# Optimization experiments

Measured on AMD Instinct MI355X. Metric: run time of the kernel, lower is better.

## Reference

```python
import jax, jax.numpy as jnp
import numpy as np

TOP_K = 30
NUM_RBF = 16
EDGE_F = 128
NODE_F = 128
MAXREL = 32
EDGE_IN = NUM_RBF * 25  # 400


def _normalize(x, eps=1e-12):
    n = jnp.linalg.norm(x, axis=-1, keepdims=True)
    return x / jnp.maximum(n, eps)


def _rbf(D):
    # D: [..., ] distances -> [..., NUM_RBF]
    mu = jnp.linspace(2.0, 22.0, NUM_RBF)
    sigma = (22.0 - 2.0) / NUM_RBF
    return jnp.exp(-(((D[..., None] - mu) / sigma) ** 2))


def _layer_norm(x, g, b, eps=1e-5):
    m = x.mean(-1, keepdims=True)
    v = ((x - m) ** 2).mean(-1, keepdims=True)
    return (x - m) / jnp.sqrt(v + eps) * g + b


def setup_inputs() -> dict:
    key = jax.random.key(0)
    ks = jax.random.split(key, 8)
    B, L = 8, 1024
    X = jax.random.normal(ks[0], (B, L, 5, 3), jnp.float32) * 3.0  # backbone coords
    mask = jnp.ones((B, L), jnp.float32)
    Lvec = jnp.full((B,), L, dtype=jnp.int32)
    W_edge = jax.random.normal(ks[1], (EDGE_IN, EDGE_F), jnp.float32) * 0.05
    W_node = jax.random.normal(ks[2], (6, NODE_F), jnp.float32) * 0.05
    W_pos = jax.random.normal(ks[3], (2 * MAXREL + 1, EDGE_F), jnp.float32) * 0.05
    b_pos = jnp.zeros((EDGE_F,), jnp.float32)
    g_edge = jnp.ones((EDGE_F,), jnp.float32)
    b_edge = jnp.zeros((EDGE_F,), jnp.float32)
    g_node = jnp.ones((NODE_F,), jnp.float32)
    b_node = jnp.zeros((NODE_F,), jnp.float32)
    return {"X": X, "mask": mask, "Lvec": Lvec, "W_edge": W_edge, "W_node": W_node,
            "W_pos": W_pos, "b_pos": b_pos, "g_edge": g_edge, "b_edge": b_edge,
            "g_node": g_node, "b_node": b_node}


def reference(X, mask, Lvec, W_edge, W_node, W_pos, b_pos, g_edge, b_edge, g_node, b_node):
    B, L = X.shape[0], X.shape[1]
    N, Ca, C, CB, O = (X[:, :, i, :] for i in range(5))

    # backbone frames (4x4: rotation rows e1,e2,e3; translation Ca; bottom row zeros)
    v1 = C - Ca
    v2 = N - Ca
    e1 = _normalize(v1)
    u2 = v2 - e1 * jnp.sum(e1 * v2, axis=-1, keepdims=True)
    e2 = _normalize(u2)
    e3 = jnp.cross(e1, e2)
    R = jnp.stack([e1, e2, e3], axis=-2)  # [B,L,3,3]
    bb = jnp.zeros((B, L, 4, 4), X.dtype).at[..., :3, :3].set(R).at[..., :3, 3].set(Ca)

    # _dist: masked Ca-Ca pairwise distance + kNN
    mask2 = mask[:, None, :] * mask[:, :, None]  # [B,L,L]
    dX = Ca[:, :, None, :] - Ca[:, None, :, :]
    D = mask2 * jnp.sqrt(jnp.sum(dX ** 2, -1) + 1e-6)
    D_max = jnp.max(D, -1, keepdims=True)
    D_adjust = D + (1.0 - mask2) * D_max
    k = min(TOP_K, L)
    negD, E_idx = jax.lax.top_k(-D_adjust, k)  # smallest-k distances
    D_neighbors = -negD  # [B,L,K]

    # RBFs: compute distances only at selected neighbors (same math as full cdist+gather)
    bidx = jnp.arange(B)[:, None, None]

    def get_rbf(A, Bc):
        Bnb = Bc[bidx, E_idx]  # [B,L,K,3]
        d = jnp.sqrt(jnp.sum((A[:, :, None, :] - Bnb) ** 2, -1) + 1e-6)
        return _rbf(d)

    pairs = [(N, N), (C, C), (O, O), (CB, CB), (Ca, N), (Ca, C), (Ca, O), (Ca, CB),
             (N, C), (N, O), (N, CB), (CB, C), (CB, O), (O, C), (N, Ca), (C, Ca),
             (O, Ca), (CB, Ca), (C, N), (O, N), (CB, N), (C, CB), (O, CB), (C, O)]
    RBF_all = jnp.concatenate([_rbf(D_neighbors)] + [get_rbf(a, b) for a, b in pairs], axis=-1)  # [B,L,K,400]

    # positional encodings over sequence offsets of selected neighbors
    offset = jnp.arange(L)[None, :, None] - E_idx  # residue_idx[i] - residue_idx[j]
    d_clip = jnp.clip(offset + MAXREL, 0, 2 * MAXREL)
    E_pos = jax.nn.one_hot(d_clip, 2 * MAXREL + 1, dtype=X.dtype) @ W_pos + b_pos

    # dihedrals (phi, psi, omega) from N/CA/C chain
    X3 = X[:, :, :3, :].reshape(B, 3 * L, 3)
    dXc = X3[:, 1:, :] - X3[:, :-1, :]
    U = _normalize(dXc)
    u_2, u_1, u_0 = U[:, :-2, :], U[:, 1:-1, :], U[:, 2:, :]
    n_2 = _normalize(jnp.cross(u_2, u_1))
    n_1 = _normalize(jnp.cross(u_1, u_0))
    cosD = jnp.clip(jnp.sum(n_2 * n_1, -1), -1 + 1e-7, 1 - 1e-7)
    Dang = jnp.sign(jnp.sum(u_2 * n_1, -1)) * jnp.arccos(cosD)
    Dang = jnp.pad(Dang, ((0, 0), (1, 2))).reshape(B, L, 3)
    V = jnp.concatenate([jnp.cos(Dang), jnp.sin(Dang)], -1)  # [B,L,6]

    E = _layer_norm(RBF_all @ W_edge + E_pos, g_edge, b_edge)
    V = _layer_norm(V @ W_node, g_node, b_node)
    return (V, E, E_idx, bb)
```

## Files before the change

kernel.cpp:

```cpp
#include <hip/hip_runtime.h>
#include <hip/hip_bf16.h>
#include <math.h>

#define V_OFF    ((size_t)0)
#define E_OFF    ((size_t)1048576)
#define EIDX_OFF ((size_t)32505856)
#define BB_OFF   ((size_t)32751616)

#define K 30
#define NRBF 16
#define AH   232
#define SSTR 132

typedef __attribute__((ext_vector_type(8))) short bf16x8;
typedef __attribute__((ext_vector_type(4))) float f32x4;

__device__ __constant__ int c_pairA[24] = {0,2,4,3,1,1,1,1,0,0,0,3,3,4,0,2,4,3,2,4,3,2,4,2};
__device__ __constant__ int c_pairB[24] = {0,2,4,3,0,2,4,3,2,4,3,2,4,2,1,1,1,1,0,0,0,3,3,4};

__device__ __constant__ float c_muS[16] = {
    1.92179871f, 3.20299785f, 4.48419699f, 5.76539613f, 7.04659527f, 8.32779441f,
    9.60899355f, 10.89019269f, 12.17139183f, 13.45259097f, 14.73379011f, 16.01498925f,
    17.29618839f, 18.57738753f, 19.85858667f, 21.13978581f};

__device__ __forceinline__ unsigned short f2bu(float f) {
    unsigned x = __float_as_uint(f);
    return (unsigned short)((x + 0x7fffu + ((x >> 16) & 1u)) >> 16);
}

__device__ __forceinline__ unsigned wave_umin64(unsigned x) {
    unsigned t;
    t = __builtin_amdgcn_update_dpp(x, x, 0x111, 0xf, 0xf, false); x = min(x, t);
    t = __builtin_amdgcn_update_dpp(x, x, 0x112, 0xf, 0xf, false); x = min(x, t);
    t = __builtin_amdgcn_update_dpp(x, x, 0x114, 0xf, 0xf, false); x = min(x, t);
    t = __builtin_amdgcn_update_dpp(x, x, 0x118, 0xf, 0xf, false); x = min(x, t);
    t = __builtin_amdgcn_update_dpp(x, x, 0x142, 0xf, 0xf, false); x = min(x, t);
    t = __builtin_amdgcn_update_dpp(x, x, 0x143, 0xf, 0xf, false); x = min(x, t);
    return (unsigned)__builtin_amdgcn_readlane((int)x, 63);
}
__device__ __forceinline__ unsigned wave_umax64(unsigned x) {
    unsigned t;
    t = __builtin_amdgcn_update_dpp(x, x, 0x111, 0xf, 0xf, false); x = max(x, t);
    t = __builtin_amdgcn_update_dpp(x, x, 0x112, 0xf, 0xf, false); x = max(x, t);
    t = __builtin_amdgcn_update_dpp(x, x, 0x114, 0xf, 0xf, false); x = max(x, t);
    t = __builtin_amdgcn_update_dpp(x, x, 0x118, 0xf, 0xf, false); x = max(x, t);
    t = __builtin_amdgcn_update_dpp(x, x, 0x142, 0xf, 0xf, false); x = max(x, t);
    t = __builtin_amdgcn_update_dpp(x, x, 0x143, 0xf, 0xf, false); x = max(x, t);
    return (unsigned)__builtin_amdgcn_readlane((int)x, 63);
}
__device__ __forceinline__ float wave_fadd64(float x) {
    float t;
    t = __int_as_float(__builtin_amdgcn_update_dpp(0, __float_as_int(x), 0x111, 0xf, 0xf, true)); x += t;
    t = __int_as_float(__builtin_amdgcn_update_dpp(0, __float_as_int(x), 0x112, 0xf, 0xf, true)); x += t;
    t = __int_as_float(__builtin_amdgcn_update_dpp(0, __float_as_int(x), 0x114, 0xf, 0xf, true)); x += t;
    t = __int_as_float(__builtin_amdgcn_update_dpp(0, __float_as_int(x), 0x118, 0xf, 0xf, true)); x += t;
    t = __int_as_float(__builtin_amdgcn_update_dpp(0, __float_as_int(x), 0x142, 0xf, 0xf, true)); x += t;
    t = __int_as_float(__builtin_amdgcn_update_dpp(0, __float_as_int(x), 0x143, 0xf, 0xf, true)); x += t;
    return __int_as_float(__builtin_amdgcn_readlane(__float_as_int(x), 63));
}
__device__ __forceinline__ unsigned mbcnt64(unsigned long long m) {
    return __builtin_amdgcn_mbcnt_hi((unsigned)(m >> 32),
           __builtin_amdgcn_mbcnt_lo((unsigned)m, 0u));
}
__device__ __forceinline__ float group8_fadd(float x) {
    float t;
    t = __int_as_float(__builtin_amdgcn_update_dpp(__float_as_int(x), __float_as_int(x), 0x0B1, 0xf, 0xf, false)); x += t;
    t = __int_as_float(__builtin_amdgcn_update_dpp(__float_as_int(x), __float_as_int(x), 0x04E, 0xf, 0xf, false)); x += t;
    x += __shfl_xor(x, 4, 64);
    return x;
}

__device__ __forceinline__ void norm_to(const float v[3], float o[3]) {
    float n = sqrtf(v[0]*v[0] + v[1]*v[1] + v[2]*v[2]);
    n = fmaxf(n, 1e-12f);
    o[0] = v[0]/n; o[1] = v[1]/n; o[2] = v[2]/n;
}
__device__ __forceinline__ void unit_diff(const float a[3], const float b[3], float o[3]) {
    float v[3] = {a[0]-b[0], a[1]-b[1], a[2]-b[2]};
    norm_to(v, o);
}
__device__ __forceinline__ void cross_unit(const float a[3], const float b[3], float o[3]) {
    float c[3] = {a[1]*b[2]-a[2]*b[1], a[2]*b[0]-a[0]*b[2], a[0]*b[1]-a[1]*b[0]};
    norm_to(c, o);
}

__global__ __launch_bounds__(128) void wb_prep_kernel(
    const float* __restrict__ We, unsigned short* __restrict__ Wb)
{
    const int s = blockIdx.x;
    const int j = threadIdx.x;
    unsigned* dst = (unsigned*)(Wb + ((size_t)(s*128 + j) << 5));
    #pragma unroll
    for (int m = 0; m < 16; ++m) {
        const int k0 = s*32 + 2*m;
        const unsigned lo = (k0   < 400) ? f2bu(We[(size_t)k0*128 + j])     : 0u;
        const unsigned hi = (k0+1 < 400) ? f2bu(We[(size_t)(k0+1)*128 + j]) : 0u;
        dst[m] = (hi << 16) | lo;
    }
}

__global__ __launch_bounds__(256) void rbf_tab_kernel(unsigned* __restrict__ tab)
{
    const int idx = blockIdx.x*256 + threadIdx.x;
    const float t1 = (idx * 0.02f) * 0.96089935f;
    unsigned* dst = tab + ((size_t)idx << 3);
    #pragma unroll
    for (int m = 0; m < 8; ++m) {
        const float z0 = t1 - c_muS[2*m];
        const float z1 = t1 - c_muS[2*m+1];
        const float v0 = exp2f(-z0*z0);
        const float v1 = exp2f(-z1*z1);
        unsigned pk;
        asm("v_cvt_pk_bf16_f32 %0, %1, %2" : "=v"(pk) : "v"(v0), "v"(v1));
        dst[m] = pk;
    }
}

__global__ __launch_bounds__(256) void ca_pack_kernel(
    const float* __restrict__ X, float4* __restrict__ ca4)
{
    const int idx = blockIdx.x*256 + threadIdx.x;
    const float* p = X + (size_t)idx*15;
    ca4[idx] = make_float4(p[3], p[4], p[5], 0.f);
}

__global__ __launch_bounds__(256, 8) void topk_edge_kernel(
    const float* __restrict__ X, const float* __restrict__ mask,
    const unsigned short* __restrict__ Wb, const float* __restrict__ Wp,
    const float* __restrict__ bp, const float* __restrict__ ge,
    const float* __restrict__ be, const float4* __restrict__ ca4,
    const unsigned* __restrict__ rtab,
    const float* __restrict__ Wn, const float* __restrict__ gn,
    const float* __restrict__ bn, float* __restrict__ out)
{
    const int blk = blockIdx.x;
    const int b = blk >> 10, i = blk & 1023;
    const int tid = threadIdx.x;
    const int w = tid >> 6, lane = tid & 63;

    __shared__ __align__(16) unsigned char uni_raw[K * SSTR * 4];
    __shared__ float redf4[4];
    __shared__ unsigned redT[4];
    __shared__ int   scount;
    __shared__ float nbA[K][15];
    __shared__ int   nj[K];
    __shared__ float dnbv[K];
    __shared__ float angf[3];
    unsigned short* A_lds = (unsigned short*)uni_raw;
    float* S = (float*)uni_raw;
    unsigned long long* surv = (unsigned long long*)uni_raw;

    if (tid == 0) scount = 0;

    const float4 me = ca4[(b << 10) + i];
    const float mi  = mask[(b << 10) + i];

    float dv_r[4], m2_r[4];
    float lmax = -1.f;
    #pragma unroll
    for (int m = 0; m < 4; ++m) {
        const int j = tid + (m << 8);
        const float4 cj = ca4[(b << 10) + j];
        const float dx = __fsub_rn(me.x, cj.x);
        const float dy = __fsub_rn(me.y, cj.y);
        const float dz = __fsub_rn(me.z, cj.z);
        const float ss = __fadd_rn(__fadd_rn(__fmul_rn(dx,dx), __fmul_rn(dy,dy)), __fmul_rn(dz,dz));
        const float dist = __fsqrt_rn(__fadd_rn(ss, 1e-6f));
        const float m2 = __fmul_rn(mi, mask[(b << 10) + j]);
        const float Dv = __fmul_rn(m2, dist);
        dv_r[m] = Dv; m2_r[m] = m2;
        lmax = fmaxf(lmax, Dv);
    }
    const float wmax = __uint_as_float(wave_umax64(__float_as_uint(lmax)));
    if (lane == 0) redf4[w] = wmax;
    __syncthreads();
    const float Dmax = fmaxf(fmaxf(redf4[0], redf4[1]), fmaxf(redf4[2], redf4[3]));

    unsigned va[4];
    #pragma unroll
    for (int m = 0; m < 4; ++m)
        va[m] = __float_as_uint(__fadd_rn(dv_r[m], __fmul_rn(__fsub_rn(1.f, m2_r[m]), Dmax)));

    {
        unsigned vb0 = va[0], vb1 = va[1], vb2 = va[2], vb3 = va[3];
        unsigned v = 0;
        #pragma unroll
        for (int k = 0; k < 8; ++k) {
            const unsigned head = min(min(vb0, vb1), min(vb2, vb3));
            v = wave_umin64(head);
            vb0 = (vb0 == v) ? 0xffffffffu : vb0;
            vb1 = (vb1 == v) ? 0xffffffffu : vb1;
            vb2 = (vb2 == v) ? 0xffffffffu : vb2;
            vb3 = (vb3 == v) ? 0xffffffffu : vb3;
        }
        if (lane == 0) redT[w] = v;
    }
    __syncthreads();
    const unsigned T = max(max(redT[0], redT[1]), max(redT[2], redT[3]));

    {
        unsigned long long mm0 = __ballot(va[0] <= T);
        unsigned long long mm1 = __ballot(va[1] <= T);
        unsigned long long mm2 = __ballot(va[2] <= T);
        unsigned long long mm3 = __ballot(va[3] <= T);
        const unsigned c0 = __popcll(mm0), c1 = __popcll(mm1);
        const unsigned c2 = __popcll(mm2), c3 = __popcll(mm3);
        int old = 0;
        if (lane == 0) old = atomicAdd(&scount, (int)(c0 + c1 + c2 + c3));
        unsigned base = (unsigned)__builtin_amdgcn_readfirstlane(old);
        if (va[0] <= T) surv[base + mbcnt64(mm0)] = ((unsigned long long)va[0] << 32) | (unsigned)tid;
        base += c0;
        if (va[1] <= T) surv[base + mbcnt64(mm1)] = ((unsigned long long)va[1] << 32) | (unsigned)(tid + 256);
        base += c1;
        if (va[2] <= T) surv[base + mbcnt64(mm2)] = ((unsigned long long)va[2] << 32) | (unsigned)(tid + 512);
        base += c2;
        if (va[3] <= T) surv[base + mbcnt64(mm3)] = ((unsigned long long)va[3] << 32) | (unsigned)(tid + 768);
    }
    __syncthreads();
    const int N = scount;

    for (int base = 0; base < N; base += 256) {
        const int t = base + tid;
        if (t < N) {
            const unsigned long long mykey = surv[t];
            int rank = 0;
            #pragma unroll 4
            for (int u = 0; u < N; ++u) rank += (surv[u] < mykey) ? 1 : 0;
            if (rank < K) {
                const int j = (int)(mykey & 0xffffffffu);
                nj[rank] = j;
                dnbv[rank] = __uint_as_float((unsigned)(mykey >> 32));
                out[EIDX_OFF + (size_t)blk * K + rank] = (float)j;
            }
        }
    }
    __syncthreads();

    for (int t = tid; t < K*15; t += 256) {
        const int e = t / 15, r = t - e*15;
        nbA[e][r] = X[((size_t)(b << 10) + nj[e])*15 + r];
    }
    __syncthreads();

    const float* sa = X + (size_t)blk * 15;
    f32x4 acc00 = {0,0,0,0}, acc01 = {0,0,0,0}, acc10 = {0,0,0,0}, acc11 = {0,0,0,0};
    const int ar = lane & 15;
    const int kg = (lane >> 4) * 8;
    const unsigned short* a_base = A_lds + ar*AH + kg;
    const unsigned short* a_base1 = a_base + 16*AH;
    const unsigned short* b_base = Wb + ((size_t)(w*32 + ar) << 5) + kg;

    for (int t = tid; t < K*12; t += 256) {
        const int e = t / 12, g = t - e*12;
        float d;
        if (g == 0) d = dnbv[e];
        else {
            const int p = g - 1;
            const int aA = c_pairA[p], aB = c_pairB[p];
            const float dx = sa[aA*3+0] - nbA[e][aB*3+0];
            const float dy = sa[aA*3+1] - nbA[e][aB*3+1];
            const float dz = sa[aA*3+2] - nbA[e][aB*3+2];
            d = sqrtf(dx*dx + dy*dy + dz*dz + 1e-6f);
        }
        int idx = (int)__fmaf_rn(d, 50.f, 0.5f);
        idx = min(idx, 4095);
        const uint4* src = (const uint4*)(rtab + ((size_t)idx << 3));
        uint4* dst = (uint4*)(A_lds + e*AH + g*NRBF);
        dst[0] = src[0]; dst[1] = src[1];
    }
    __syncthreads();
    #pragma unroll
    for (int s = 0; s < 6; ++s) {
        const bf16x8 a0 = *reinterpret_cast<const bf16x8*>(a_base + s*32);
        const bf16x8 a1 = *reinterpret_cast<const bf16x8*>(a_base1 + s*32);
        const bf16x8 b0 = *reinterpret_cast<const bf16x8*>(b_base + (size_t)s*4096);
        const bf16x8 b1 = *reinterpret_cast<const bf16x8*>(b_base + (size_t)s*4096 + 512);
        acc00 = __builtin_amdgcn_mfma_f32_16x16x32_bf16(a0, b0, acc00, 0, 0, 0);
        acc01 = __builtin_amdgcn_mfma_f32_16x16x32_bf16(a0, b1, acc01, 0, 0, 0);
        acc10 = __builtin_amdgcn_mfma_f32_16x16x32_bf16(a1, b0, acc10, 0, 0, 0);
        acc11 = __builtin_amdgcn_mfma_f32_16x16x32_bf16(a1, b1, acc11, 0, 0, 0);
    }
    __syncthreads();

    for (int t = tid; t < K*13; t += 256) {
        const int e = t / 13, gg = t - e*13;
        const int p = 11 + gg;
        const int aA = c_pairA[p], aB = c_pairB[p];
        const float dx = sa[aA*3+0] - nbA[e][aB*3+0];
        const float dy = sa[aA*3+1] - nbA[e][aB*3+1];
        const float dz = sa[aA*3+2] - nbA[e][aB*3+2];
        const float d = sqrtf(dx*dx + dy*dy + dz*dz + 1e-6f);
        int idx = (int)__fmaf_rn(d, 50.f, 0.5f);
        idx = min(idx, 4095);
        const uint4* src = (const uint4*)(rtab + ((size_t)idx << 3));
        uint4* dst = (uint4*)(A_lds + e*AH + gg*NRBF);
        dst[0] = src[0]; dst[1] = src[1];
    }
    for (int t = tid; t < K*8; t += 256) {
        const int e = t >> 3, c = t & 7;
        ((unsigned*)(A_lds + e*AH + 208))[c] = 0u;
    }
    __syncthreads();
    #pragma unroll
    for (int s = 0; s < 7; ++s) {
        const bf16x8 a0 = *reinterpret_cast<const bf16x8*>(a_base + s*32);
        const bf16x8 a1 = *reinterpret_cast<const bf16x8*>(a_base1 + s*32);
        const bf16x8 b0 = *reinterpret_cast<const bf16x8*>(b_base + (size_t)(6+s)*4096);
        const bf16x8 b1 = *reinterpret_cast<const bf16x8*>(b_base + (size_t)(6+s)*4096 + 512);
        acc00 = __builtin_amdgcn_mfma_f32_16x16x32_bf16(a0, b0, acc00, 0, 0, 0);
        acc01 = __builtin_amdgcn_mfma_f32_16x16x32_bf16(a0, b1, acc01, 0, 0, 0);
        acc10 = __builtin_amdgcn_mfma_f32_16x16x32_bf16(a1, b0, acc10, 0, 0, 0);
        acc11 = __builtin_amdgcn_mfma_f32_16x16x32_bf16(a1, b1, acc11, 0, 0, 0);
    }
    __syncthreads();

    {
        const int crow = (lane >> 4) * 4;
        const int ccol = w*32 + (lane & 15);
        #pragma unroll
        for (int r = 0; r < 4; ++r) {
            const int r0 = crow + r;
            if (r0 < K) { S[r0*SSTR + ccol] = acc00[r]; S[r0*SSTR + ccol + 16] = acc01[r]; }
            const int r1 = 16 + crow + r;
            if (r1 < K) { S[r1*SSTR + ccol] = acc10[r]; S[r1*SSTR + ccol + 16] = acc11[r]; }
        }
    }
    __syncthreads();

    {
        const int e = tid >> 3, s8 = tid & 7;
        if (e < K) {
            int off = i - nj[e] + 32;
            off = off < 0 ? 0 : (off > 64 ? 64 : off);
            const int j0 = s8*16;
            const float* row = S + e*SSTR + j0;
            const float* wpr = Wp + (size_t)off*128 + j0;
            const float* bpr = bp + j0;
            float xv[16];
            float sum = 0.f;
            #pragma unroll
            for (int c = 0; c < 4; ++c) {
                const float4 q  = ((const float4*)row)[c];
                const float4 wp = ((const float4*)wpr)[c];
                const float4 bq = ((const float4*)bpr)[c];
                const float v0 = q.x + (wp.x + bq.x);
                const float v1 = q.y + (wp.y + bq.y);
                const float v2 = q.z + (wp.z + bq.z);
                const float v3 = q.w + (wp.w + bq.w);
                xv[4*c+0] = v0; xv[4*c+1] = v1; xv[4*c+2] = v2; xv[4*c+3] = v3;
                sum += v0 + v1 + v2 + v3;
            }
            const float mean = group8_fadd(sum) * (1.f/128.f);
            float vs = 0.f;
            #pragma unroll
            for (int c = 0; c < 16; ++c) { const float d = xv[c] - mean; xv[c] = d; vs = __fmaf_rn(d, d, vs); }
            const float inv = 1.f / __fsqrt_rn(group8_fadd(vs) * (1.f/128.f) + 1e-5f);
            float* op = out + E_OFF + ((size_t)blk * K + e) * 128 + j0;
            #pragma unroll
            for (int c = 0; c < 4; ++c) {
                const float4 g4 = ((const float4*)(ge + j0))[c];
                const float4 b4 = ((const float4*)(be + j0))[c];
                float4 o;
                o.x = xv[4*c+0] * inv * g4.x + b4.x;
                o.y = xv[4*c+1] * inv * g4.y + b4.y;
                o.z = xv[4*c+2] * inv * g4.z + b4.z;
                o.w = xv[4*c+3] * inv * g4.w + b4.w;
                ((float4*)op)[c] = o;
            }
        }
    }

    if (tid < 3) {
        const int m = 3*i + tid;
        float dang = 0.f;
        if (m >= 1 && m <= 3*1024 - 3) {
            const int t = m - 1;
            float P[4][3];
            #pragma unroll
            for (int q = 0; q < 4; ++q) {
                const int s = t + q;
                const int ri = s / 3, ai = s - 3*ri;
                const float* p = X + (((size_t)b * 1024 + ri) * 5 + ai) * 3;
                P[q][0] = p[0]; P[q][1] = p[1]; P[q][2] = p[2];
            }
            float u2v[3], u1v[3], u0v[3];
            unit_diff(P[1], P[0], u2v);
            unit_diff(P[2], P[1], u1v);
            unit_diff(P[3], P[2], u0v);
            float n2v[3], n1v[3];
            cross_unit(u2v, u1v, n2v);
            cross_unit(u1v, u0v, n1v);
            float cosD = n2v[0]*n1v[0] + n2v[1]*n1v[1] + n2v[2]*n1v[2];
            cosD = fminf(fmaxf(cosD, -1.f + 1e-7f), 1.f - 1e-7f);
            float sg = u2v[0]*n1v[0] + u2v[1]*n1v[1] + u2v[2]*n1v[2];
            float s = (sg > 0.f) ? 1.f : ((sg < 0.f) ? -1.f : 0.f);
            dang = s * acosf(cosD);
        }
        angf[tid] = dang;
    }
    if (tid == 3) {
        float Nx=sa[0],  Ny=sa[1],  Nz=sa[2];
        float Cax=sa[3], Cay=sa[4], Caz=sa[5];
        float Cx=sa[6],  Cy=sa[7],  Cz=sa[8];
        float v1[3] = {Cx-Cax, Cy-Cay, Cz-Caz};
        float v2[3] = {Nx-Cax, Ny-Cay, Nz-Caz};
        float e1[3]; norm_to(v1, e1);
        float dd = e1[0]*v2[0] + e1[1]*v2[1] + e1[2]*v2[2];
        float u2[3] = {v2[0]-e1[0]*dd, v2[1]-e1[1]*dd, v2[2]-e1[2]*dd};
        float e2[3]; norm_to(u2, e2);
        float e3[3] = {e1[1]*e2[2]-e1[2]*e2[1], e1[2]*e2[0]-e1[0]*e2[2], e1[0]*e2[1]-e1[1]*e2[0]};
        float* bb = out + BB_OFF + (size_t)blk * 16;
        bb[0]=e1[0]; bb[1]=e1[1]; bb[2]=e1[2];  bb[3]=Cax;
        bb[4]=e2[0]; bb[5]=e2[1]; bb[6]=e2[2];  bb[7]=Cay;
        bb[8]=e3[0]; bb[9]=e3[1]; bb[10]=e3[2]; bb[11]=Caz;
        bb[12]=0.f; bb[13]=0.f; bb[14]=0.f; bb[15]=0.f;
    }
    __syncthreads();
    float xV = 0.f;
    if (tid < 128) {
        const float a0 = angf[0], a1 = angf[1], a2 = angf[2];
        const float feat[6] = {cosf(a0), cosf(a1), cosf(a2), sinf(a0), sinf(a1), sinf(a2)};
        #pragma unroll
        for (int f = 0; f < 6; ++f) xV += feat[f] * Wn[f*128 + tid];
        const float s = wave_fadd64(xV);
        if (lane == 0) redf4[w] = s;
    }
    __syncthreads();
    float xm = 0.f;
    if (tid < 128) {
        const float mean = (redf4[0] + redf4[1]) * (1.f/128.f);
        xm = xV - mean;
        const float vsum = wave_fadd64(xm*xm);
        if (lane == 0) redT[w] = __float_as_uint(vsum);
    }
    __syncthreads();
    if (tid < 128) {
        const float var = (__uint_as_float(redT[0]) + __uint_as_float(redT[1])) * (1.f/128.f);
        out[V_OFF + (size_t)blk * 128 + tid] = xm / __fsqrt_rn(var + 1e-5f) * gn[tid] + bn[tid];
    }
}

extern "C" void kernel_launch(void* const* d_in, const int* in_sizes, int n_in,
                              void* d_out, int out_size, void* d_ws, size_t ws_size,
                              hipStream_t stream) {
    const float* X    = (const float*)d_in[0];
    const float* mask = (const float*)d_in[1];
    const float* We   = (const float*)d_in[3];
    const float* Wn   = (const float*)d_in[4];
    const float* Wp   = (const float*)d_in[5];
    const float* bp   = (const float*)d_in[6];
    const float* gE   = (const float*)d_in[7];
    const float* bE   = (const float*)d_in[8];
    const float* gN   = (const float*)d_in[9];
    const float* bN   = (const float*)d_in[10];
    float* out = (float*)d_out;
    unsigned short* Wb = (unsigned short*)d_ws;
    float4* ca4 = (float4*)((char*)d_ws + 106496);
    unsigned* rtab = (unsigned*)((char*)d_ws + 106496 + 131072);

    hipLaunchKernelGGL(wb_prep_kernel,   dim3(13),   dim3(128), 0, stream, We, Wb);
    hipLaunchKernelGGL(rbf_tab_kernel,   dim3(16),   dim3(256), 0, stream, rtab);
    hipLaunchKernelGGL(ca_pack_kernel,   dim3(32),   dim3(256), 0, stream, X, ca4);
    hipLaunchKernelGGL(topk_edge_kernel, dim3(8192), dim3(256), 0, stream,
                       X, mask, Wb, Wp, bp, gE, bE, ca4, rtab, Wn, gN, bN, out);
}
```

Measured before the change: 146.0 us.

## Prefetch positional rows early, split threshold min-search, use DPP in group reduce

The W_pos rows for each neighbour are now loaded into registers right after the neighbour indices are known, so their global latency overlaps the RBF build and MFMA loop instead of stalling the layer-norm epilogue. The per-wave 8th-smallest search becomes two independent 4-round min chains over halves of the candidates, which shortens the serial reduction chain; the threshold is the max of the two results, which is still a valid upper bound but may let more survivors through. The xor-4 shuffle in the 8-lane reduction is replaced by a DPP row operation. The prefetch holds 16 extra registers live across the matmul, which may reduce occupancy.

```diff
diff --git a/kernel.cpp b/kernel.cpp
--- a/kernel.cpp
+++ b/kernel.cpp
@@ -66,7 +66,7 @@
     float t;
     t = __int_as_float(__builtin_amdgcn_update_dpp(__float_as_int(x), __float_as_int(x), 0x0B1, 0xf, 0xf, false)); x += t;
     t = __int_as_float(__builtin_amdgcn_update_dpp(__float_as_int(x), __float_as_int(x), 0x04E, 0xf, 0xf, false)); x += t;
-    x += __shfl_xor(x, 4, 64);
+    t = __int_as_float(__builtin_amdgcn_update_dpp(__float_as_int(x), __float_as_int(x), 0x141, 0xf, 0xf, false)); x += t;
     return x;
 }
 
@@ -182,18 +182,21 @@
         va[m] = __float_as_uint(__fadd_rn(dv_r[m], __fmul_rn(__fsub_rn(1.f, m2_r[m]), Dmax)));
 
     {
-        unsigned vb0 = va[0], vb1 = va[1], vb2 = va[2], vb3 = va[3];
-        unsigned v = 0;
-        #pragma unroll
-        for (int k = 0; k < 8; ++k) {
-            const unsigned head = min(min(vb0, vb1), min(vb2, vb3));
-            v = wave_umin64(head);
-            vb0 = (vb0 == v) ? 0xffffffffu : vb0;
-            vb1 = (vb1 == v) ? 0xffffffffu : vb1;
-            vb2 = (vb2 == v) ? 0xffffffffu : vb2;
-            vb3 = (vb3 == v) ? 0xffffffffu : vb3;
-        }
-        if (lane == 0) redT[w] = v;
+        unsigned a0 = va[0], a1 = va[1];
+        unsigned b0 = va[2], b1 = va[3];
+        unsigned vA = 0, vB = 0;
+        #pragma unroll
+        for (int k = 0; k < 4; ++k) {
+            const unsigned hA = min(a0, a1);
+            const unsigned hB = min(b0, b1);
+            vA = wave_umin64(hA);
+            vB = wave_umin64(hB);
+            a0 = (a0 == vA) ? 0xffffffffu : a0;
+            a1 = (a1 == vA) ? 0xffffffffu : a1;
+            b0 = (b0 == vB) ? 0xffffffffu : b0;
+            b1 = (b1 == vB) ? 0xffffffffu : b1;
+        }
+        if (lane == 0) redT[w] = max(vA, vB);
     }
     __syncthreads();
     const unsigned T = max(max(redT[0], redT[1]), max(redT[2], redT[3]));
@@ -236,6 +239,16 @@
     }
     __syncthreads();
 
+    const int eL = tid >> 3, j0L = (tid & 7) * 16;
+    float4 wp4[4];
+    if (eL < K) {
+        int off = i - nj[eL] + 32;
+        off = off < 0 ? 0 : (off > 64 ? 64 : off);
+        const float* wpr = Wp + (size_t)off*128 + j0L;
+        #pragma unroll
+        for (int c = 0; c < 4; ++c) wp4[c] = ((const float4*)wpr)[c];
+    }
+
     for (int t = tid; t < K*15; t += 256) {
         const int e = t / 15, r = t - e*15;
         nbA[e][r] = X[((size_t)(b << 10) + nj[e])*15 + r];
@@ -327,46 +340,39 @@
     }
     __syncthreads();
 
-    {
-        const int e = tid >> 3, s8 = tid & 7;
-        if (e < K) {
-            int off = i - nj[e] + 32;
-            off = off < 0 ? 0 : (off > 64 ? 64 : off);
-            const int j0 = s8*16;
-            const float* row = S + e*SSTR + j0;
-            const float* wpr = Wp + (size_t)off*128 + j0;
-            const float* bpr = bp + j0;
-            float xv[16];
-            float sum = 0.f;
-            #pragma unroll
-            for (int c = 0; c < 4; ++c) {
-                const float4 q  = ((const float4*)row)[c];
-                const float4 wp = ((const float4*)wpr)[c];
-                const float4 bq = ((const float4*)bpr)[c];
-                const float v0 = q.x + (wp.x + bq.x);
-                const float v1 = q.y + (wp.y + bq.y);
-                const float v2 = q.z + (wp.z + bq.z);
-                const float v3 = q.w + (wp.w + bq.w);
-                xv[4*c+0] = v0; xv[4*c+1] = v1; xv[4*c+2] = v2; xv[4*c+3] = v3;
-                sum += v0 + v1 + v2 + v3;
-            }
-            const float mean = group8_fadd(sum) * (1.f/128.f);
-            float vs = 0.f;
-            #pragma unroll
-            for (int c = 0; c < 16; ++c) { const float d = xv[c] - mean; xv[c] = d; vs = __fmaf_rn(d, d, vs); }
-            const float inv = 1.f / __fsqrt_rn(group8_fadd(vs) * (1.f/128.f) + 1e-5f);
-            float* op = out + E_OFF + ((size_t)blk * K + e) * 128 + j0;
-            #pragma unroll
-            for (int c = 0; c < 4; ++c) {
-                const float4 g4 = ((const float4*)(ge + j0))[c];
-                const float4 b4 = ((const float4*)(be + j0))[c];
-                float4 o;
-                o.x = xv[4*c+0] * inv * g4.x + b4.x;
-                o.y = xv[4*c+1] * inv * g4.y + b4.y;
-                o.z = xv[4*c+2] * inv * g4.z + b4.z;
-                o.w = xv[4*c+3] * inv * g4.w + b4.w;
-                ((float4*)op)[c] = o;
-            }
+    if (eL < K) {
+        const float* row = S + eL*SSTR + j0L;
+        const float* bpr = bp + j0L;
+        float xv[16];
+        float sum = 0.f;
+        #pragma unroll
+        for (int c = 0; c < 4; ++c) {
+            const float4 q  = ((const float4*)row)[c];
+            const float4 wp = wp4[c];
+            const float4 bq = ((const float4*)bpr)[c];
+            const float v0 = q.x + (wp.x + bq.x);
+            const float v1 = q.y + (wp.y + bq.y);
+            const float v2 = q.z + (wp.z + bq.z);
+            const float v3 = q.w + (wp.w + bq.w);
+            xv[4*c+0] = v0; xv[4*c+1] = v1; xv[4*c+2] = v2; xv[4*c+3] = v3;
+            sum += v0 + v1 + v2 + v3;
+        }
+        const float mean = group8_fadd(sum) * (1.f/128.f);
+        float vs = 0.f;
+        #pragma unroll
+        for (int c = 0; c < 16; ++c) { const float d = xv[c] - mean; xv[c] = d; vs = __fmaf_rn(d, d, vs); }
+        const float inv = 1.f / __fsqrt_rn(group8_fadd(vs) * (1.f/128.f) + 1e-5f);
+        float* op = out + E_OFF + ((size_t)blk * K + eL) * 128 + j0L;
+        #pragma unroll
+        for (int c = 0; c < 4; ++c) {
+            const float4 g4 = ((const float4*)(ge + j0L))[c];
+            const float4 b4 = ((const float4*)(be + j0L))[c];
+            float4 o;
+            o.x = xv[4*c+0] * inv * g4.x + b4.x;
+            o.y = xv[4*c+1] * inv * g4.y + b4.y;
+            o.z = xv[4*c+2] * inv * g4.z + b4.z;
+            o.w = xv[4*c+3] * inv * g4.w + b4.w;
+            ((float4*)op)[c] = o;
         }
     }
 
```

Measured after the change: 156.7 us. +7.3%, slower.
